# Performance work log

Hardware: AMD Instinct MI355X
Metric: run time of the kernel (lower is better)

The kernel has to match this reference:

```python
import jax, jax.numpy as jnp
import numpy as np

DEGREE = 8
D = 512
K = 256
O = 512
N = 65536


def setup_inputs() -> dict:
    key = jax.random.key(0)
    ks = jax.random.split(key, 4)
    z = jax.random.normal(ks[0], (N, D), dtype=jnp.float32)
    T0 = jnp.ones((K,), dtype=jnp.float32)
    # T[i-1] corresponds to parameter T_i, i = 1..DEGREE, each [K, D]
    T = jax.random.normal(ks[1], (DEGREE, K, D), dtype=jnp.float32) * 0.02
    C_w = jax.random.normal(ks[2], (O, K), dtype=jnp.float32) * (1.0 / np.sqrt(K))
    C_b = jnp.zeros((O,), dtype=jnp.float32)
    return {"z": z, "T0": T0, "T": T, "C_w": C_w, "C_b": C_b}


def reference(z, T0, T, C_w, C_b):
    # z: [N, D]; T: [DEGREE, K, D]; recurrence over polynomial degree n:
    #   out_n = (z @ ((2n-1)/n * T_n).T) * out_{n-1} - (n-1)/n * out_{n-2}
    z = z.reshape(-1, D)
    out_prev2 = T0                                  # degree 0, [K] (broadcasts over N)
    out_prev1 = jnp.einsum('nd,kd->nk', z, T[0])    # degree 1, [N, K]
    for n in range(2, DEGREE + 1):
        a = (2.0 * n - 1.0) / n
        b = (n - 1.0) / n
        cur = jnp.einsum('nd,kd->nk', z, a * T[n - 1]) * out_prev1 - b * out_prev2
        out_prev2, out_prev1 = out_prev1, cur
    # layer_C applied to out_list[degree]
    return out_prev1 @ C_w.T + C_b
```

## Files before the change

### kernel.cpp

```cpp
#include <hip/hip_runtime.h>
#include <hip/hip_fp16.h>
#include <cstdint>

#define NROWS 65536
#define DIM   512
#define KDIM  256
#define ODIM  512
#define DEG   8
#define ZN    (NROWS * DIM)
#define TN    (DEG * KDIM * DIM)
#define CWN   (ODIM * KDIM)

typedef _Float16 f16x8 __attribute__((ext_vector_type(8)));
typedef float    f32x4 __attribute__((ext_vector_type(4)));


__device__ __forceinline__ void gld_lds16(const void* g, void* l) {
  __builtin_amdgcn_global_load_lds(
      (const __attribute__((address_space(1))) unsigned int*)g,
      (__attribute__((address_space(3))) unsigned int*)l, 16, 0, 0);
}

__device__ __forceinline__ unsigned pack2h(float a, float b) {
  union { _Float16 h[2]; unsigned u; } x;
  x.h[0] = (_Float16)a; x.h[1] = (_Float16)b;
  return x.u;
}

__device__ __forceinline__ int swz(int row, int chunk) {
  return (row << 7) | (((chunk + row) & 7) << 4);
}


__global__ void k_convert(const float* __restrict__ z,
                          const float* __restrict__ T,
                          const float* __restrict__ Cw,
                          _Float16* __restrict__ z16,
                          _Float16* __restrict__ Tb,
                          _Float16* __restrict__ Cwb) {
  long e = ((long)blockIdx.x * 256 + threadIdx.x) * 4;
  const float* src;
  _Float16* dst;
  float s = 1.0f;
  if (e < ZN) {
    src = z + e; dst = z16 + e;
  } else {
    long o = e - ZN;
    if (o < TN) {
      int n = (int)(o >> 17);
      s = (n == 0) ? 1.0f : (float)(2 * n + 1) / (float)(n + 1);
      src = T + o; dst = Tb + o;
    } else {
      long c = o - TN;
      if (c >= CWN) return;
      src = Cw + c; dst = Cwb + c;
    }
  }
  float4 v = *(const float4*)src;
  uint2 p; p.x = pack2h(v.x * s, v.y * s); p.y = pack2h(v.z * s, v.w * s);
  *(uint2*)dst = p;
}


__launch_bounds__(256, 3)
__global__ void k_poly(const _Float16* __restrict__ z16,
                       const float* __restrict__ T0,
                       const _Float16* __restrict__ Tb,
                       _Float16* __restrict__ u8) {
  __shared__ __align__(16) uint16_t As[128 * 64];
  __shared__ __align__(16) uint16_t Bs[128 * 64];

  const int tid = threadIdx.x;
  const int wave = tid >> 6, lane = tid & 63;

  const int id = blockIdx.x;
  const int super = id >> 8, rem = id & 255;
  const int kg = rem >> 4;
  const int rt = (super << 4) | (rem & 15);
  const int r0 = rt << 7;
  const int k0 = kg << 4;

  const int m_l = lane & 15, kq = lane >> 4;
  const int wrow = wave << 5;

  f32x4 acc[DEG][2];
#pragma unroll
  for (int n = 0; n < DEG; n++)
#pragma unroll
    for (int a = 0; a < 2; a++)
      acc[n][a] = (f32x4){0.f, 0.f, 0.f, 0.f};

  const _Float16* aptr[4];
  const _Float16* bptr[4];
  int lofs[4];
#pragma unroll
  for (int j = 0; j < 4; j++) {
    int lin = (j << 8) + tid;
    int row = lin >> 3;
    int c = ((lin & 7) - row) & 7;
    lofs[j] = lin << 4;
    aptr[j] = z16 + (size_t)(r0 + row) * DIM + (c << 3);
    int n = row >> 4, kk = row & 15;
    bptr[j] = Tb + (size_t)((n << 8) + k0 + kk) * DIM + (c << 3);
  }

  for (int it = 0; it < DIM / 64; it++) {
    __syncthreads();
#pragma unroll
    for (int j = 0; j < 4; j++) gld_lds16(aptr[j], (char*)As + lofs[j]);
#pragma unroll
    for (int j = 0; j < 4; j++) gld_lds16(bptr[j], (char*)Bs + lofs[j]);
#pragma unroll
    for (int j = 0; j < 4; j++) { aptr[j] += 64; bptr[j] += 64; }
    __syncthreads();

#pragma unroll
    for (int ks = 0; ks < 2; ks++) {
      const int chunk = (ks << 2) + kq;
      f16x8 af[2];
#pragma unroll
      for (int mf = 0; mf < 2; mf++)
        af[mf] = *(const f16x8*)((char*)As + swz(wrow + (mf << 4) + m_l, chunk));
#pragma unroll
      for (int n = 0; n < DEG; n++) {
        f16x8 bv = *(const f16x8*)((char*)Bs + swz((n << 4) + m_l, chunk));
#pragma unroll
        for (int mf = 0; mf < 2; mf++)
          acc[n][mf] = __builtin_amdgcn_mfma_f32_16x16x32_f16(
              af[mf], bv, acc[n][mf], 0, 0, 0);
      }
    }
  }

  const float bcoef[7] = {1.f/2.f, 2.f/3.f, 3.f/4.f, 4.f/5.f,
                          5.f/6.f, 6.f/7.f, 7.f/8.f};
  const int col = k0 + m_l;
  const float t0v = T0[col];
#pragma unroll
  for (int mf = 0; mf < 2; mf++) {
    f32x4 up2 = {t0v, t0v, t0v, t0v};
    f32x4 up1 = acc[0][mf];
#pragma unroll
    for (int n = 2; n <= DEG; n++) {
      f32x4 cur = acc[n - 1][mf] * up1 - bcoef[n - 2] * up2;
      up2 = up1; up1 = cur;
    }
    const int rbase = r0 + wrow + (mf << 4) + (kq << 2);
#pragma unroll
    for (int r = 0; r < 4; r++)
      u8[(size_t)(rbase + r) * KDIM + col] = (_Float16)up1[r];
  }
}


__launch_bounds__(256, 4)
__global__ void k_out(const _Float16* __restrict__ u8,
                      const _Float16* __restrict__ Cwb,
                      const float* __restrict__ Cb,
                      float* __restrict__ out) {
  __shared__ __align__(16) uint16_t As[128 * 64];
  __shared__ __align__(16) uint16_t Bs[64 * 64];

  const int tid = threadIdx.x;
  const int wave = tid >> 6, lane = tid & 63;

  const int id = blockIdx.x;
  const int super = id >> 7, rem = id & 127;
  const int cg = rem >> 4;
  const int rt = (super << 4) | (rem & 15);
  const int r0 = rt << 7;
  const int c0 = cg << 6;

  const int m_l = lane & 15, kq = lane >> 4;
  const int wrow = wave << 5;

  f32x4 acc[2][4];
#pragma unroll
  for (int a = 0; a < 2; a++)
#pragma unroll
    for (int b = 0; b < 4; b++)
      acc[a][b] = (f32x4){0.f, 0.f, 0.f, 0.f};

  const _Float16* aptr[4];
  const _Float16* bptr[2];
  int lofsA[4], lofsB[2];
#pragma unroll
  for (int j = 0; j < 4; j++) {
    int lin = (j << 8) + tid;
    int row = lin >> 3;
    int c = ((lin & 7) - row) & 7;
    lofsA[j] = lin << 4;
    aptr[j] = u8 + (size_t)(r0 + row) * KDIM + (c << 3);
  }
#pragma unroll
  for (int j = 0; j < 2; j++) {
    int lin = (j << 8) + tid;
    int row = lin >> 3;
    int c = ((lin & 7) - row) & 7;
    lofsB[j] = lin << 4;
    bptr[j] = Cwb + (size_t)(c0 + row) * KDIM + (c << 3);
  }

  for (int it = 0; it < KDIM / 64; it++) {
    __syncthreads();
#pragma unroll
    for (int j = 0; j < 4; j++) gld_lds16(aptr[j], (char*)As + lofsA[j]);
#pragma unroll
    for (int j = 0; j < 2; j++) gld_lds16(bptr[j], (char*)Bs + lofsB[j]);
#pragma unroll
    for (int j = 0; j < 4; j++) aptr[j] += 64;
#pragma unroll
    for (int j = 0; j < 2; j++) bptr[j] += 64;
    __syncthreads();

#pragma unroll
    for (int ks = 0; ks < 2; ks++) {
      const int chunk = (ks << 2) + kq;
      f16x8 af[2];
#pragma unroll
      for (int mf = 0; mf < 2; mf++)
        af[mf] = *(const f16x8*)((char*)As + swz(wrow + (mf << 4) + m_l, chunk));
#pragma unroll
      for (int kf = 0; kf < 4; kf++) {
        f16x8 bv = *(const f16x8*)((char*)Bs + swz((kf << 4) + m_l, chunk));
#pragma unroll
        for (int mf = 0; mf < 2; mf++)
          acc[mf][kf] = __builtin_amdgcn_mfma_f32_16x16x32_f16(
              af[mf], bv, acc[mf][kf], 0, 0, 0);
      }
    }
  }

#pragma unroll
  for (int kf = 0; kf < 4; kf++) {
    const int col = c0 + (kf << 4) + m_l;
    const float cb = Cb[col];
#pragma unroll
    for (int mf = 0; mf < 2; mf++) {
      const int rbase = r0 + wrow + (mf << 4) + (kq << 2);
#pragma unroll
      for (int r = 0; r < 4; r++)
        out[(size_t)(rbase + r) * ODIM + col] = acc[mf][kf][r] + cb;
    }
  }
}


extern "C" void kernel_launch(void* const* d_in, const int* in_sizes, int n_in,
                              void* d_out, int out_size, void* d_ws, size_t ws_size,
                              hipStream_t stream) {
  const float* z  = (const float*)d_in[0];
  const float* T0 = (const float*)d_in[1];
  const float* T  = (const float*)d_in[2];
  const float* Cw = (const float*)d_in[3];
  const float* Cb = (const float*)d_in[4];
  float* out = (float*)d_out;

  char* ws = (char*)d_ws;
  _Float16* z16 = (_Float16*)ws;
  _Float16* Tb  = (_Float16*)(ws + (size_t)ZN * 2);
  _Float16* Cwb = (_Float16*)(ws + (size_t)ZN * 2 + (size_t)TN * 2);
  _Float16* u8  = (_Float16*)(ws + (size_t)ZN * 2 + (size_t)TN * 2 + (size_t)CWN * 2);

  k_convert<<<33920, 256, 0, stream>>>(z, T, Cw, z16, Tb, Cwb);
  k_poly<<<8192, 256, 0, stream>>>(z16, T0, Tb, u8);
  k_out<<<4096, 256, 0, stream>>>(u8, Cwb, Cb, out);
}
```

Measured before the change: 390.6 us.

## Fuse z fp32-to-fp16 conversion into poly GEMM with register prefetch and double-buffered B

Removes the separate pass that converts z to fp16. k_poly now loads fp32 z into registers, packs it to fp16, and writes it into swizzled LDS. The next tile of z is prefetched into registers and the next T tile goes into a second LDS buffer, so loads overlap the MFMA work. Block indices are also remapped so neighbouring row tiles land on the same XCD for L2 locality. The cost is that z is read as fp32 by each of the 16 k-group blocks, doubling z traffic per block, plus more registers and LDS per block.

Result: slower. 414.2 us (+6.0%).

```diff
diff --git a/kernel.cpp b/kernel.cpp
--- a/kernel.cpp
+++ b/kernel.cpp
@@ -7,7 +7,6 @@
 #define KDIM  256
 #define ODIM  512
 #define DEG   8
-#define ZN    (NROWS * DIM)
 #define TN    (DEG * KDIM * DIM)
 #define CWN   (ODIM * KDIM)
 
@@ -32,29 +31,22 @@
 }
 
 
-__global__ void k_convert(const float* __restrict__ z,
-                          const float* __restrict__ T,
+__global__ void k_convert(const float* __restrict__ T,
                           const float* __restrict__ Cw,
-                          _Float16* __restrict__ z16,
                           _Float16* __restrict__ Tb,
                           _Float16* __restrict__ Cwb) {
   long e = ((long)blockIdx.x * 256 + threadIdx.x) * 4;
   const float* src;
   _Float16* dst;
   float s = 1.0f;
-  if (e < ZN) {
-    src = z + e; dst = z16 + e;
+  if (e < TN) {
+    int n = (int)(e >> 17);
+    s = (n == 0) ? 1.0f : (float)(2 * n + 1) / (float)(n + 1);
+    src = T + e; dst = Tb + e;
   } else {
-    long o = e - ZN;
-    if (o < TN) {
-      int n = (int)(o >> 17);
-      s = (n == 0) ? 1.0f : (float)(2 * n + 1) / (float)(n + 1);
-      src = T + o; dst = Tb + o;
-    } else {
-      long c = o - TN;
-      if (c >= CWN) return;
-      src = Cw + c; dst = Cwb + c;
-    }
+    long c = e - TN;
+    if (c >= CWN) return;
+    src = Cw + c; dst = Cwb + c;
   }
   float4 v = *(const float4*)src;
   uint2 p; p.x = pack2h(v.x * s, v.y * s); p.y = pack2h(v.z * s, v.w * s);
@@ -63,20 +55,21 @@
 
 
 __launch_bounds__(256, 3)
-__global__ void k_poly(const _Float16* __restrict__ z16,
+__global__ void k_poly(const float* __restrict__ z,
                        const float* __restrict__ T0,
                        const _Float16* __restrict__ Tb,
                        _Float16* __restrict__ u8) {
   __shared__ __align__(16) uint16_t As[128 * 64];
-  __shared__ __align__(16) uint16_t Bs[128 * 64];
+  __shared__ __align__(16) uint16_t Bs[2][128 * 64];
 
   const int tid = threadIdx.x;
   const int wave = tid >> 6, lane = tid & 63;
 
   const int id = blockIdx.x;
-  const int super = id >> 8, rem = id & 255;
-  const int kg = rem >> 4;
-  const int rt = (super << 4) | (rem & 15);
+  const int xcd = id & 7;
+  const int s = id >> 3;
+  const int kg = s & 15;
+  const int rt = (xcd << 6) | (s >> 4);
   const int r0 = rt << 7;
   const int k0 = kg << 4;
 
@@ -90,29 +83,62 @@
     for (int a = 0; a < 2; a++)
       acc[n][a] = (f32x4){0.f, 0.f, 0.f, 0.f};
 
-  const _Float16* aptr[4];
   const _Float16* bptr[4];
-  int lofs[4];
+  int lofsB[4];
 #pragma unroll
   for (int j = 0; j < 4; j++) {
     int lin = (j << 8) + tid;
     int row = lin >> 3;
     int c = ((lin & 7) - row) & 7;
-    lofs[j] = lin << 4;
-    aptr[j] = z16 + (size_t)(r0 + row) * DIM + (c << 3);
+    lofsB[j] = lin << 4;
     int n = row >> 4, kk = row & 15;
     bptr[j] = Tb + (size_t)((n << 8) + k0 + kk) * DIM + (c << 3);
   }
 
+  const int arow = tid >> 4;
+  const int ac = tid & 15;
+  const float* abase = z + (size_t)(r0 + arow) * DIM + (ac << 2);
+  int aofs[8];
+#pragma unroll
+  for (int j = 0; j < 8; j++) {
+    int row = (j << 4) + arow;
+    aofs[j] = (row << 7) | ((((ac >> 1) + row) & 7) << 4) | ((ac & 1) << 3);
+  }
+
+  float4 rA[8];
+#pragma unroll
+  for (int j = 0; j < 8; j++)
+    rA[j] = *(const float4*)(abase + (size_t)(j << 4) * DIM);
+#pragma unroll
+  for (int j = 0; j < 4; j++) gld_lds16(bptr[j], (char*)Bs[0] + lofsB[j]);
+
   for (int it = 0; it < DIM / 64; it++) {
-    __syncthreads();
-#pragma unroll
-    for (int j = 0; j < 4; j++) gld_lds16(aptr[j], (char*)As + lofs[j]);
-#pragma unroll
-    for (int j = 0; j < 4; j++) gld_lds16(bptr[j], (char*)Bs + lofs[j]);
-#pragma unroll
-    for (int j = 0; j < 4; j++) { aptr[j] += 64; bptr[j] += 64; }
-    __syncthreads();
+    const int cur = it & 1;
+    asm volatile("s_waitcnt vmcnt(0)" ::: "memory");
+    __builtin_amdgcn_sched_barrier(0);
+    __builtin_amdgcn_s_barrier();
+
+#pragma unroll
+    for (int j = 0; j < 8; j++) {
+      uint2 p;
+      p.x = pack2h(rA[j].x, rA[j].y);
+      p.y = pack2h(rA[j].z, rA[j].w);
+      *(uint2*)((char*)As + aofs[j]) = p;
+    }
+
+    if (it < DIM / 64 - 1) {
+#pragma unroll
+      for (int j = 0; j < 8; j++)
+        rA[j] = *(const float4*)(abase + ((it + 1) << 6) +
+                                 (size_t)(j << 4) * DIM);
+#pragma unroll
+      for (int j = 0; j < 4; j++)
+        gld_lds16(bptr[j] + ((it + 1) << 6), (char*)Bs[cur ^ 1] + lofsB[j]);
+    }
+
+    asm volatile("s_waitcnt lgkmcnt(0)" ::: "memory");
+    __builtin_amdgcn_sched_barrier(0);
+    __builtin_amdgcn_s_barrier();
 
 #pragma unroll
     for (int ks = 0; ks < 2; ks++) {
@@ -123,7 +149,7 @@
         af[mf] = *(const f16x8*)((char*)As + swz(wrow + (mf << 4) + m_l, chunk));
 #pragma unroll
       for (int n = 0; n < DEG; n++) {
-        f16x8 bv = *(const f16x8*)((char*)Bs + swz((n << 4) + m_l, chunk));
+        f16x8 bv = *(const f16x8*)((char*)Bs[cur] + swz((n << 4) + m_l, chunk));
 #pragma unroll
         for (int mf = 0; mf < 2; mf++)
           acc[n][mf] = __builtin_amdgcn_mfma_f32_16x16x32_f16(
@@ -165,9 +191,10 @@
   const int wave = tid >> 6, lane = tid & 63;
 
   const int id = blockIdx.x;
-  const int super = id >> 7, rem = id & 127;
-  const int cg = rem >> 4;
-  const int rt = (super << 4) | (rem & 15);
+  const int xcd = id & 7;
+  const int s = id >> 3;
+  const int cg = s & 7;
+  const int rt = (xcd << 6) | (s >> 3);
   const int r0 = rt << 7;
   const int c0 = cg << 6;
 
@@ -257,12 +284,11 @@
   float* out = (float*)d_out;
 
   char* ws = (char*)d_ws;
-  _Float16* z16 = (_Float16*)ws;
-  _Float16* Tb  = (_Float16*)(ws + (size_t)ZN * 2);
-  _Float16* Cwb = (_Float16*)(ws + (size_t)ZN * 2 + (size_t)TN * 2);
-  _Float16* u8  = (_Float16*)(ws + (size_t)ZN * 2 + (size_t)TN * 2 + (size_t)CWN * 2);
-
-  k_convert<<<33920, 256, 0, stream>>>(z, T, Cw, z16, Tb, Cwb);
-  k_poly<<<8192, 256, 0, stream>>>(z16, T0, Tb, u8);
+  _Float16* Tb  = (_Float16*)ws;
+  _Float16* Cwb = (_Float16*)(ws + (size_t)TN * 2);
+  _Float16* u8  = (_Float16*)(ws + (size_t)TN * 2 + (size_t)CWN * 2);
+
+  k_convert<<<1152, 256, 0, stream>>>(T, Cw, Tb, Cwb);
+  k_poly<<<8192, 256, 0, stream>>>(z, T0, Tb, u8);
   k_out<<<4096, 256, 0, stream>>>(u8, Cwb, Cb, out);
 }
```

## Double-buffer one GEMM operand in LDS and remap k_out blocks per XCD

Applied to the files above, without the earlier changes.

Both GEMM kernels now double-buffer one operand in shared memory: Tb tiles in k_poly and u8 tiles in k_out. The next tile is prefetched with global_load_lds while the current one is consumed, and explicit s_waitcnt/s_barrier replace __syncthreads. The aim is to hide global load latency behind MFMA work. k_out also remaps block IDs so that consecutive row tiles land on the same XCD, which should improve L2 reuse of Cwb and u8. The extra LDS (48KB in k_poly) may lower occupancy, and the vmcnt(4) accounting assumes a fixed number of outstanding loads.

After: 377.7 us. 3.3% less time.

```diff
diff --git a/kernel.cpp b/kernel.cpp
--- a/kernel.cpp
+++ b/kernel.cpp
@@ -68,7 +68,7 @@
                        const _Float16* __restrict__ Tb,
                        _Float16* __restrict__ u8) {
   __shared__ __align__(16) uint16_t As[128 * 64];
-  __shared__ __align__(16) uint16_t Bs[128 * 64];
+  __shared__ __align__(16) uint16_t Bs[2][128 * 64];
 
   const int tid = threadIdx.x;
   const int wave = tid >> 6, lane = tid & 63;
@@ -104,15 +104,35 @@
     bptr[j] = Tb + (size_t)((n << 8) + k0 + kk) * DIM + (c << 3);
   }
 
+#pragma unroll
+  for (int j = 0; j < 4; j++) gld_lds16(bptr[j], (char*)Bs[0] + lofs[j]);
+#pragma unroll
+  for (int j = 0; j < 4; j++) bptr[j] += 64;
+
   for (int it = 0; it < DIM / 64; it++) {
-    __syncthreads();
+    const int cur = it & 1;
+    __builtin_amdgcn_sched_barrier(0);
+    __builtin_amdgcn_s_barrier();
+    __builtin_amdgcn_sched_barrier(0);
+
 #pragma unroll
     for (int j = 0; j < 4; j++) gld_lds16(aptr[j], (char*)As + lofs[j]);
 #pragma unroll
-    for (int j = 0; j < 4; j++) gld_lds16(bptr[j], (char*)Bs + lofs[j]);
-#pragma unroll
-    for (int j = 0; j < 4; j++) { aptr[j] += 64; bptr[j] += 64; }
-    __syncthreads();
+    for (int j = 0; j < 4; j++) aptr[j] += 64;
+
+    if (it < DIM / 64 - 1) {
+#pragma unroll
+      for (int j = 0; j < 4; j++)
+        gld_lds16(bptr[j], (char*)Bs[cur ^ 1] + lofs[j]);
+#pragma unroll
+      for (int j = 0; j < 4; j++) bptr[j] += 64;
+      asm volatile("s_waitcnt vmcnt(4)" ::: "memory");
+    } else {
+      asm volatile("s_waitcnt vmcnt(0)" ::: "memory");
+    }
+    __builtin_amdgcn_sched_barrier(0);
+    __builtin_amdgcn_s_barrier();
+    __builtin_amdgcn_sched_barrier(0);
 
 #pragma unroll
     for (int ks = 0; ks < 2; ks++) {
@@ -123,7 +143,7 @@
         af[mf] = *(const f16x8*)((char*)As + swz(wrow + (mf << 4) + m_l, chunk));
 #pragma unroll
       for (int n = 0; n < DEG; n++) {
-        f16x8 bv = *(const f16x8*)((char*)Bs + swz((n << 4) + m_l, chunk));
+        f16x8 bv = *(const f16x8*)((char*)Bs[cur] + swz((n << 4) + m_l, chunk));
 #pragma unroll
         for (int mf = 0; mf < 2; mf++)
           acc[n][mf] = __builtin_amdgcn_mfma_f32_16x16x32_f16(
@@ -158,16 +178,17 @@
                       const _Float16* __restrict__ Cwb,
                       const float* __restrict__ Cb,
                       float* __restrict__ out) {
-  __shared__ __align__(16) uint16_t As[128 * 64];
+  __shared__ __align__(16) uint16_t As[2][128 * 64];
   __shared__ __align__(16) uint16_t Bs[64 * 64];
 
   const int tid = threadIdx.x;
   const int wave = tid >> 6, lane = tid & 63;
 
   const int id = blockIdx.x;
-  const int super = id >> 7, rem = id & 127;
-  const int cg = rem >> 4;
-  const int rt = (super << 4) | (rem & 15);
+  const int xcd = id & 7;
+  const int s = id >> 3;
+  const int cg = s & 7;
+  const int rt = (xcd << 6) | (s >> 3);
   const int r0 = rt << 7;
   const int c0 = cg << 6;
 
@@ -201,17 +222,35 @@
     bptr[j] = Cwb + (size_t)(c0 + row) * KDIM + (c << 3);
   }
 
+#pragma unroll
+  for (int j = 0; j < 4; j++) gld_lds16(aptr[j], (char*)As[0] + lofsA[j]);
+#pragma unroll
+  for (int j = 0; j < 4; j++) aptr[j] += 64;
+
   for (int it = 0; it < KDIM / 64; it++) {
-    __syncthreads();
-#pragma unroll
-    for (int j = 0; j < 4; j++) gld_lds16(aptr[j], (char*)As + lofsA[j]);
+    const int cur = it & 1;
+    __builtin_amdgcn_sched_barrier(0);
+    __builtin_amdgcn_s_barrier();
+    __builtin_amdgcn_sched_barrier(0);
+
 #pragma unroll
     for (int j = 0; j < 2; j++) gld_lds16(bptr[j], (char*)Bs + lofsB[j]);
 #pragma unroll
-    for (int j = 0; j < 4; j++) aptr[j] += 64;
-#pragma unroll
     for (int j = 0; j < 2; j++) bptr[j] += 64;
-    __syncthreads();
+
+    if (it < KDIM / 64 - 1) {
+#pragma unroll
+      for (int j = 0; j < 4; j++)
+        gld_lds16(aptr[j], (char*)As[cur ^ 1] + lofsA[j]);
+#pragma unroll
+      for (int j = 0; j < 4; j++) aptr[j] += 64;
+      asm volatile("s_waitcnt vmcnt(4)" ::: "memory");
+    } else {
+      asm volatile("s_waitcnt vmcnt(0)" ::: "memory");
+    }
+    __builtin_amdgcn_sched_barrier(0);
+    __builtin_amdgcn_s_barrier();
+    __builtin_amdgcn_sched_barrier(0);
 
 #pragma unroll
     for (int ks = 0; ks < 2; ks++) {
@@ -219,7 +258,7 @@
       f16x8 af[2];
 #pragma unroll
       for (int mf = 0; mf < 2; mf++)
-        af[mf] = *(const f16x8*)((char*)As + swz(wrow + (mf << 4) + m_l, chunk));
+        af[mf] = *(const f16x8*)((char*)As[cur] + swz(wrow + (mf << 4) + m_l, chunk));
 #pragma unroll
       for (int kf = 0; kf < 4; kf++) {
         f16x8 bv = *(const f16x8*)((char*)Bs + swz((kf << 4) + m_l, chunk));
```
